# Kernel optimization log

Measured on AMD Instinct MI355X. Metric: run time of the kernel, lower is better.

Reference implementation:

```python
import jax, jax.numpy as jnp
import numpy as np

B, Q, K, D = 32, 1024, 1024, 128

def setup_inputs() -> dict:
    key = jax.random.key(0)
    kq, kk, kv, kl = jax.random.split(key, 4)
    return {
        "queries": jax.random.normal(kq, (B, Q, D), dtype=jnp.float32),
        "keys": jax.random.normal(kk, (B, K, D), dtype=jnp.float32),
        "values": jax.random.normal(kv, (B, K, D), dtype=jnp.float32),
        "valid_length": jax.random.randint(kl, (B,), 1, K + 1),
    }

def reference(queries, keys, values, valid_length):
    d = queries.shape[-1]
    # scores: [B, Q, K]
    scores = jnp.einsum("bqd,bkd->bqk", queries, keys) / jnp.sqrt(jnp.float32(d))
    # length mask: position k is valid iff k < valid_length[b]
    mask = jnp.arange(keys.shape[1])[None, None, :] < valid_length[:, None, None]
    scores = jnp.where(mask, scores, jnp.float32(-1e9))
    attn = jax.nn.softmax(scores, axis=-1)
    # dropout module is identity in eval / p=0
    return jnp.einsum("bqk,bkv->bqv", attn, values)
```

## Files before the change

### kernel.cpp

```cpp
#include <hip/hip_runtime.h>
#include <hip/hip_bf16.h>
#include <stdint.h>

#define B_    32
#define QLEN  1024
#define KSEQ  1024
#define DIM   128
#define NKT   (KSEQ / 64)
#define SCALE 0.08838834764831845f

typedef __attribute__((ext_vector_type(8))) short  short8;
typedef __attribute__((ext_vector_type(4))) float  floatx4;
typedef unsigned int u32;

__device__ __forceinline__ u32 f2bf(float x) {
  union { float f; u32 u; } v; v.f = x;
  return (v.u + 0x7FFF + ((v.u >> 16) & 1)) >> 16;
}
__device__ __forceinline__ u32 pack2(float lo, float hi) {
  return f2bf(lo) | (f2bf(hi) << 16);
}

__device__ __forceinline__ void barrier_full() {
  asm volatile("s_waitcnt vmcnt(0) lgkmcnt(0)" ::: "memory");
  __syncthreads();
}

__global__ __launch_bounds__(256) void prep_kernel(const float* __restrict__ Kg,
                                                   const float* __restrict__ Vg,
                                                   const int* __restrict__ vlen,
                                                   uint4* __restrict__ Ksw,
                                                   uint4* __restrict__ Vsw) {
  const int kt = blockIdx.x, b = blockIdx.y, t = threadIdx.x;
  if (kt * 64 >= vlen[b]) return;
  if (blockIdx.z == 0) {
    const float* src = Kg + ((size_t)b * KSEQ + kt * 64) * DIM;
    uint4* dst = Ksw + ((size_t)b * NKT + kt) * 1024;
#pragma unroll
    for (int it = 0; it < 4; it++) {
      const int f = it * 256 + t, r = f >> 4, c = f & 15;
      floatx4 f0 = *(const floatx4*)(src + r * DIM + c * 8);
      floatx4 f1 = *(const floatx4*)(src + r * DIM + c * 8 + 4);
      uint4 o;
      o.x = pack2(f0[0], f0[1]); o.y = pack2(f0[2], f0[3]);
      o.z = pack2(f1[0], f1[1]); o.w = pack2(f1[2], f1[3]);
      dst[r * 16 + (c ^ (r & 15))] = o;
    }
  } else {
    const float* src = Vg + ((size_t)b * KSEQ + kt * 64) * DIM;
    uint4* dst = Vsw + ((size_t)b * NKT + kt) * 1024;
#pragma unroll
    for (int it = 0; it < 4; it++) {
      const int id = it * 256 + t, d = id & 127, kc = id >> 7;
      float v[8];
#pragma unroll
      for (int j = 0; j < 8; j++) v[j] = src[(size_t)(kc * 8 + j) * DIM + d];
      uint4 o;
      o.x = pack2(v[0], v[1]); o.y = pack2(v[2], v[3]);
      o.z = pack2(v[4], v[5]); o.w = pack2(v[6], v[7]);
      dst[d * 8 + (kc ^ (d & 7))] = o;
    }
  }
}

typedef const __attribute__((address_space(1))) u32* as1p;
typedef __attribute__((address_space(3))) u32* as3p;
__device__ __forceinline__ void gl_lds16(const void* g, void* l) {
  __builtin_amdgcn_global_load_lds((as1p)g, (as3p)l, 16, 0, 0);
}

__global__ __launch_bounds__(256, 2) void attn_kernel(
    const float* __restrict__ Qg, const uint4* __restrict__ Ksw,
    const uint4* __restrict__ Vsw, const int* __restrict__ vlen,
    float* __restrict__ Og) {
  __shared__ __align__(16) short Kbuf[2][64 * 128];
  __shared__ __align__(16) short Vbuf[2][128 * 64];
  __shared__ __align__(16) short Pl[4][16][72];

  const int b = blockIdx.x, q0 = blockIdx.y * 64;
  const int t = threadIdx.x, wave = t >> 6, lane = t & 63;
  const int quad = lane >> 4, m = lane & 15;
  const int L  = vlen[b];
  const int nt = (L + 63) >> 6;

  const char* Kt = (const char*)(Ksw + (size_t)b * NKT * 1024);
  const char* Vt = (const char*)(Vsw + (size_t)b * NKT * 1024);

  short8 aq[4];
  {
    const float* qrow = Qg + ((size_t)b * QLEN + q0 + wave * 16 + m) * DIM;
#pragma unroll
    for (int c = 0; c < 4; c++) {
      floatx4 f0 = *(const floatx4*)(qrow + c * 32 + quad * 8);
      floatx4 f1 = *(const floatx4*)(qrow + c * 32 + quad * 8 + 4);
      short8 a;
      a[0] = (short)f2bf(f0[0]); a[1] = (short)f2bf(f0[1]);
      a[2] = (short)f2bf(f0[2]); a[3] = (short)f2bf(f0[3]);
      a[4] = (short)f2bf(f1[0]); a[5] = (short)f2bf(f1[1]);
      a[6] = (short)f2bf(f1[2]); a[7] = (short)f2bf(f1[3]);
      aq[c] = a;
    }
  }

  float lrow[4];
  floatx4 oacc[8];
#pragma unroll
  for (int r = 0; r < 4; r++) lrow[r] = 0.0f;
#pragma unroll
  for (int d = 0; d < 8; d++) oacc[d] = (floatx4){0.f, 0.f, 0.f, 0.f};

#define ISSUE_K(tk, bb)                                                        \
  {                                                                            \
    const char* g_ = Kt + (size_t)(tk) * 16384 + wave * 4096 + lane * 16;      \
    _Pragma("unroll") for (int i_ = 0; i_ < 4; i_++)                           \
        gl_lds16(g_ + i_ * 1024, (char*)Kbuf[bb] + wave * 4096 + i_ * 1024);   \
  }
#define ISSUE_V(tk, bb)                                                        \
  {                                                                            \
    const char* g_ = Vt + (size_t)(tk) * 16384 + wave * 4096 + lane * 16;      \
    _Pragma("unroll") for (int i_ = 0; i_ < 4; i_++)                           \
        gl_lds16(g_ + i_ * 1024, (char*)Vbuf[bb] + wave * 4096 + i_ * 1024);   \
  }

  ISSUE_K(0, 0);
  ISSUE_V(0, 0);

  for (int tk = 0; tk < nt; tk++) {
    const int k0 = tk * 64;
    barrier_full();
    if (tk + 1 < nt) {
      ISSUE_K(tk + 1, (tk + 1) & 1);
      ISSUE_V(tk + 1, (tk + 1) & 1);
    }
    const short* Kb_ = Kbuf[tk & 1];
    const short* Vb_ = Vbuf[tk & 1];

    floatx4 sa[4];
#pragma unroll
    for (int s = 0; s < 4; s++) sa[s] = (floatx4){0.f, 0.f, 0.f, 0.f};
#pragma unroll
    for (int s = 0; s < 4; s++) {
#pragma unroll
      for (int c = 0; c < 4; c++) {
        const short8 bk = *(const short8*)(Kb_ + (s * 16 + m) * 128 +
                                           (((c * 4 + quad) ^ m) & 15) * 8);
        sa[s] = __builtin_amdgcn_mfma_f32_16x16x32_bf16(aq[c], bk, sa[s], 0, 0, 0);
      }
    }

    float p[4][4];
    if (k0 + 64 <= L) {
#pragma unroll
      for (int s = 0; s < 4; s++)
#pragma unroll
        for (int r = 0; r < 4; r++)
          p[s][r] = __expf(fminf(sa[s][r] * SCALE, 30.0f));
    } else {
      const bool vv[4] = {(k0 + m) < L, (k0 + 16 + m) < L,
                          (k0 + 32 + m) < L, (k0 + 48 + m) < L};
#pragma unroll
      for (int s = 0; s < 4; s++)
#pragma unroll
        for (int r = 0; r < 4; r++)
          p[s][r] = vv[s] ? __expf(fminf(sa[s][r] * SCALE, 30.0f)) : 0.0f;
    }
#pragma unroll
    for (int r = 0; r < 4; r++)
      lrow[r] += (p[0][r] + p[1][r]) + (p[2][r] + p[3][r]);

#pragma unroll
    for (int s = 0; s < 4; s++) {
#pragma unroll
      for (int r = 0; r < 4; r++)
        Pl[wave][quad * 4 + r][s * 16 + m] = (short)f2bf(p[s][r]);
    }
    asm volatile("s_waitcnt lgkmcnt(0)" ::: "memory");
    const short8 pa0 = *(const short8*)&Pl[wave][m][quad * 8];
    const short8 pa1 = *(const short8*)&Pl[wave][m][32 + quad * 8];

#pragma unroll
    for (int d = 0; d < 8; d++) {
      const int row = d * 16 + m;
      const short8 bv0 = *(const short8*)(Vb_ + row * 64 + ((quad ^ (m & 7)) & 7) * 8);
      const short8 bv1 = *(const short8*)(Vb_ + row * 64 + (((quad + 4) ^ (m & 7)) & 7) * 8);
      oacc[d] = __builtin_amdgcn_mfma_f32_16x16x32_bf16(pa0, bv0, oacc[d], 0, 0, 0);
      oacc[d] = __builtin_amdgcn_mfma_f32_16x16x32_bf16(pa1, bv1, oacc[d], 0, 0, 0);
    }
  }

#pragma unroll
  for (int off = 1; off < 16; off <<= 1) {
#pragma unroll
    for (int r = 0; r < 4; r++) lrow[r] += __shfl_xor(lrow[r], off);
  }
  float inv[4];
#pragma unroll
  for (int r = 0; r < 4; r++) inv[r] = 1.0f / lrow[r];
  float* orow = Og + ((size_t)b * QLEN + q0 + wave * 16) * DIM;
#pragma unroll
  for (int d = 0; d < 8; d++) {
#pragma unroll
    for (int r = 0; r < 4; r++)
      orow[(size_t)(quad * 4 + r) * DIM + d * 16 + m] = oacc[d][r] * inv[r];
  }
#undef ISSUE_K
#undef ISSUE_V
}

extern "C" void kernel_launch(void* const* d_in, const int* in_sizes, int n_in,
                              void* d_out, int out_size, void* d_ws, size_t ws_size,
                              hipStream_t stream) {
  const float* Qg = (const float*)d_in[0];
  const float* Kg = (const float*)d_in[1];
  const float* Vg = (const float*)d_in[2];
  const int*  vln = (const int*)d_in[3];
  uint4* Ksw = (uint4*)d_ws;
  uint4* Vsw = (uint4*)((char*)d_ws + (size_t)B_ * NKT * 16384);

  prep_kernel<<<dim3(NKT, B_, 2), 256, 0, stream>>>(Kg, Vg, vln, Ksw, Vsw);
  attn_kernel<<<dim3(B_, QLEN / 64), 256, 0, stream>>>(Qg, Ksw, Vsw, vln,
                                                       (float*)d_out);
}
```

Baseline: 121.9 us.

## Schedule attention blocks longest-batch-first via device-side task table

Adds a single-block scheduling kernel that sorts batches by number of valid key tiles and writes a task table, so the attention grid becomes a 1-D list of (batch, query-block) tasks. The order interleaves long and short batches across ranks to balance work over CUs, cutting tail imbalance caused by variable valid lengths. The cost is an extra tiny serial kernel launch and one indirect load per block.

Result: slower. 217.6 us (+78.5%).

```diff
diff --git a/kernel.cpp b/kernel.cpp
--- a/kernel.cpp
+++ b/kernel.cpp
@@ -63,6 +63,30 @@
   }
 }
 
+__global__ __launch_bounds__(256) void sched_kernel(const int* __restrict__ vlen,
+                                                    int2* __restrict__ task) {
+  __shared__ int sidx[32];
+  if (threadIdx.x == 0) {
+    int nt[32], idx[32];
+    for (int b = 0; b < 32; b++) { nt[b] = (vlen[b] + 63) >> 6; idx[b] = b; }
+    for (int i = 0; i < 31; i++) {
+      int m = i;
+      for (int j = i + 1; j < 32; j++)
+        if (nt[idx[j]] > nt[idx[m]]) m = j;
+      int t = idx[i]; idx[i] = idx[m]; idx[m] = t;
+    }
+    for (int i = 0; i < 32; i++) sidx[i] = idx[i];
+  }
+  __syncthreads();
+  for (int l = threadIdx.x; l < 512; l += 256) {
+    const int x = l & 7, j = l >> 3;
+    int rank, q;
+    if (j < 32) { rank = (j & 1) ? x + 8  : x;      q = j >> 1; }
+    else        { rank = (j & 1) ? x + 16 : x + 24; q = (j - 32) >> 1; }
+    task[l] = make_int2(sidx[rank], q << 6);
+  }
+}
+
 typedef const __attribute__((address_space(1))) u32* as1p;
 typedef __attribute__((address_space(3))) u32* as3p;
 __device__ __forceinline__ void gl_lds16(const void* g, void* l) {
@@ -72,12 +96,13 @@
 __global__ __launch_bounds__(256, 2) void attn_kernel(
     const float* __restrict__ Qg, const uint4* __restrict__ Ksw,
     const uint4* __restrict__ Vsw, const int* __restrict__ vlen,
-    float* __restrict__ Og) {
+    const int2* __restrict__ task, float* __restrict__ Og) {
   __shared__ __align__(16) short Kbuf[2][64 * 128];
   __shared__ __align__(16) short Vbuf[2][128 * 64];
   __shared__ __align__(16) short Pl[4][16][72];
 
-  const int b = blockIdx.x, q0 = blockIdx.y * 64;
+  const int2 tq = task[blockIdx.x];
+  const int b = tq.x, q0 = tq.y;
   const int t = threadIdx.x, wave = t >> 6, lane = t & 63;
   const int quad = lane >> 4, m = lane & 15;
   const int L  = vlen[b];
@@ -216,8 +241,10 @@
   const int*  vln = (const int*)d_in[3];
   uint4* Ksw = (uint4*)d_ws;
   uint4* Vsw = (uint4*)((char*)d_ws + (size_t)B_ * NKT * 16384);
-
+  int2*  Tsk = (int2*)((char*)d_ws + 2 * (size_t)B_ * NKT * 16384);
+
+  sched_kernel<<<1, 256, 0, stream>>>(vln, Tsk);
   prep_kernel<<<dim3(NKT, B_, 2), 256, 0, stream>>>(Kg, Vg, vln, Ksw, Vsw);
-  attn_kernel<<<dim3(B_, QLEN / 64), 256, 0, stream>>>(Qg, Ksw, Vsw, vln,
-                                                       (float*)d_out);
-}
+  attn_kernel<<<dim3(512), 256, 0, stream>>>(Qg, Ksw, Vsw, vln, Tsk,
+                                             (float*)d_out);
+}
```
